# Optimization experiments

Hardware: AMD Instinct MI355X
Metric: run time of the kernel (lower is better)

Reference implementation:

```python
import jax, jax.numpy as jnp
import numpy as np
import math

VOCAB = 32000
DIM = 1024
TOKENS = 4096
PAD_IDX = 0
NBITS = 4
QN = -(2 ** (NBITS - 1))        # -8
QP = 2 ** (NBITS - 1) - 1       # 7


def setup_inputs() -> dict:
    key = jax.random.key(0)
    k_idx, k_w = jax.random.split(key)
    idx = jax.random.randint(k_idx, (TOKENS,), 0, VOCAB)
    # x is one-hot over the vocabulary, as implied by topk(x,1)[1] extracting the index
    x = jax.nn.one_hot(idx, VOCAB, dtype=jnp.float32)
    weight = jax.random.normal(k_w, (DIM, VOCAB), dtype=jnp.float32) * 0.02
    # LSQ init rule: alpha = 2 * mean|W| / sqrt(Qp)
    alpha = (2.0 * jnp.mean(jnp.abs(weight)) / math.sqrt(QP)).reshape(1)
    return {"x": x, "weight": weight, "alpha": alpha}


def reference(x, weight, alpha):
    # topk(x, 1)[1] on a one-hot input == argmax over vocab
    idx = jnp.argmax(x, axis=-1)                       # [T]
    mask = (idx == PAD_IDX)[:, None]                   # [T, 1]
    a = alpha[0]
    # LSQ fake-quantize the weight: round(clamp(w/alpha, Qn, Qp)) * alpha
    w_q = jnp.round(jnp.clip(weight / a, QN, QP)) * a  # [DIM, VOCAB]
    out = jnp.einsum('tv,dv->td', x, w_q)              # [T, DIM]
    return jnp.where(mask, 0.0, out)
```

## Files before the change

### kernel.cpp

```cpp
#include <hip/hip_runtime.h>


constexpr int VOCAB  = 32000;
constexpr int DIM    = 1024;
constexpr int TOKENS = 4096;
constexpr int V4     = VOCAB / 4;
constexpr int BLOCK  = 256;

__global__ __launch_bounds__(BLOCK) void emb_lsq_kernel(
    const float* __restrict__ x,
    const float* __restrict__ w,
    const float* __restrict__ alpha,
    float* __restrict__ out)
{
    const int t   = blockIdx.x;
    const int tid = threadIdx.x;

    __shared__ volatile int s_idx;
    if (tid == 0) s_idx = -1;
    __syncthreads();

    const float4* xr = reinterpret_cast<const float4*>(x + (size_t)t * VOCAB);
    for (int i = tid; i < V4; i += BLOCK) {
        float4 v = xr[i];
        int found = -1;
        if      (v.x > 0.5f) found = 4 * i + 0;
        else if (v.y > 0.5f) found = 4 * i + 1;
        else if (v.z > 0.5f) found = 4 * i + 2;
        else if (v.w > 0.5f) found = 4 * i + 3;
        if (found >= 0) s_idx = found;
        if (s_idx >= 0) break;
    }
    __syncthreads();
    const int idx = s_idx;

    float* orow = out + (size_t)t * DIM;
    if (idx == 0) {
        for (int d = tid; d < DIM; d += BLOCK) orow[d] = 0.0f;
    } else {
        const float a = alpha[0];
        for (int d = tid; d < DIM; d += BLOCK) {
            float wv = w[(size_t)d * VOCAB + idx];
            float q  = rintf(fminf(fmaxf(wv / a, -8.0f), 7.0f)) * a;
            orow[d]  = q;
        }
    }
}

extern "C" void kernel_launch(void* const* d_in, const int* in_sizes, int n_in,
                              void* d_out, int out_size, void* d_ws, size_t ws_size,
                              hipStream_t stream) {
    const float* x     = (const float*)d_in[0];
    const float* w     = (const float*)d_in[1];
    const float* alpha = (const float*)d_in[2];
    float* out         = (float*)d_out;

    emb_lsq_kernel<<<TOKENS, BLOCK, 0, stream>>>(x, w, alpha, out);
}
```

Before: 733.7 us.

## Use one wavefront per token with ballot-based early exit and unrolled loads

Each token is now handled by a single 64-lane wavefront instead of a 256-thread block. The one-hot search uses four-way unrolled vector loads per lane and a wave ballot for early exit, replacing the shared-memory flag and block barriers. The gather of weight values is unrolled into 16 independent loads per lane, and the output is written with vector stores. The aim is to drop synchronization overhead and get more memory-level parallelism per lane. The cost is fewer threads per token, so the scan over the x row gets less parallelism within each token.

```diff
diff --git a/kernel.cpp b/kernel.cpp
--- a/kernel.cpp
+++ b/kernel.cpp
@@ -1,48 +1,80 @@
 #include <hip/hip_runtime.h>
 
+
+typedef float v4f __attribute__((ext_vector_type(4)));
 
 constexpr int VOCAB  = 32000;
 constexpr int DIM    = 1024;
 constexpr int TOKENS = 4096;
 constexpr int V4     = VOCAB / 4;
-constexpr int BLOCK  = 256;
+constexpr int WAVE   = 64;
+constexpr int FULL_ITERS = V4 / 256;
+constexpr int TAIL_BASE  = FULL_ITERS * 256;
 
-__global__ __launch_bounds__(BLOCK) void emb_lsq_kernel(
+__device__ __forceinline__ int check4(v4f v, int chunk) {
+    if (v.x > 0.5f) return 4 * chunk + 0;
+    if (v.y > 0.5f) return 4 * chunk + 1;
+    if (v.z > 0.5f) return 4 * chunk + 2;
+    if (v.w > 0.5f) return 4 * chunk + 3;
+    return -1;
+}
+
+__global__ __launch_bounds__(WAVE) void emb_lsq_kernel(
     const float* __restrict__ x,
     const float* __restrict__ w,
     const float* __restrict__ alpha,
     float* __restrict__ out)
 {
-    const int t   = blockIdx.x;
-    const int tid = threadIdx.x;
+    const int t    = blockIdx.x;
+    const int lane = threadIdx.x;
 
-    __shared__ volatile int s_idx;
-    if (tid == 0) s_idx = -1;
-    __syncthreads();
+    const v4f* xr = reinterpret_cast<const v4f*>(x + (size_t)t * VOCAB);
+    int found = -1;
+    for (int k = 0; k < FULL_ITERS; ++k) {
+        const int i = lane + 256 * k;
+        v4f a0 = xr[i];
+        v4f a1 = xr[i +  64];
+        v4f a2 = xr[i + 128];
+        v4f a3 = xr[i + 192];
+        int f;
+        if ((f = check4(a0, i      )) >= 0) found = f;
+        else if ((f = check4(a1, i +  64)) >= 0) found = f;
+        else if ((f = check4(a2, i + 128)) >= 0) found = f;
+        else if ((f = check4(a3, i + 192)) >= 0) found = f;
+        if (__ballot(found >= 0)) break;
+    }
+    if (!__ballot(found >= 0)) {
+        v4f a = xr[TAIL_BASE + lane];
+        found = check4(a, TAIL_BASE + lane);
+    }
+    unsigned long long m = __ballot(found >= 0);
+    const int idx = m ? __shfl(found, (int)__ffsll(m) - 1) : -1;
 
-    const float4* xr = reinterpret_cast<const float4*>(x + (size_t)t * VOCAB);
-    for (int i = tid; i < V4; i += BLOCK) {
-        float4 v = xr[i];
-        int found = -1;
-        if      (v.x > 0.5f) found = 4 * i + 0;
-        else if (v.y > 0.5f) found = 4 * i + 1;
-        else if (v.z > 0.5f) found = 4 * i + 2;
-        else if (v.w > 0.5f) found = 4 * i + 3;
-        if (found >= 0) s_idx = found;
-        if (s_idx >= 0) break;
-    }
-    __syncthreads();
-    const int idx = s_idx;
-
-    float* orow = out + (size_t)t * DIM;
-    if (idx == 0) {
-        for (int d = tid; d < DIM; d += BLOCK) orow[d] = 0.0f;
+    v4f* orow = reinterpret_cast<v4f*>(out + (size_t)t * DIM);
+    if (idx <= 0) {
+        v4f z = 0.f;
+        #pragma unroll
+        for (int j = 0; j < 4; ++j) orow[lane + 64 * j] = z;
     } else {
         const float a = alpha[0];
-        for (int d = tid; d < DIM; d += BLOCK) {
-            float wv = w[(size_t)d * VOCAB + idx];
-            float q  = rintf(fminf(fmaxf(wv / a, -8.0f), 7.0f)) * a;
-            orow[d]  = q;
+        const size_t col = (size_t)idx;
+        float wv[16];
+        #pragma unroll
+        for (int j = 0; j < 4; ++j) {
+            const int d0 = 4 * lane + 256 * j;
+            wv[4*j+0] = w[(size_t)(d0 + 0) * VOCAB + col];
+            wv[4*j+1] = w[(size_t)(d0 + 1) * VOCAB + col];
+            wv[4*j+2] = w[(size_t)(d0 + 2) * VOCAB + col];
+            wv[4*j+3] = w[(size_t)(d0 + 3) * VOCAB + col];
+        }
+        #pragma unroll
+        for (int j = 0; j < 4; ++j) {
+            v4f q;
+            q.x = rintf(fminf(fmaxf(wv[4*j+0] / a, -8.f), 7.f)) * a;
+            q.y = rintf(fminf(fmaxf(wv[4*j+1] / a, -8.f), 7.f)) * a;
+            q.z = rintf(fminf(fmaxf(wv[4*j+2] / a, -8.f), 7.f)) * a;
+            q.w = rintf(fminf(fmaxf(wv[4*j+3] / a, -8.f), 7.f)) * a;
+            orow[lane + 64 * j] = q;
         }
     }
 }
@@ -55,5 +87,5 @@
     const float* alpha = (const float*)d_in[2];
     float* out         = (float*)d_out;
 
-    emb_lsq_kernel<<<TOKENS, BLOCK, 0, stream>>>(x, w, alpha, out);
+    emb_lsq_kernel<<<TOKENS, WAVE, 0, stream>>>(x, w, alpha, out);
 }
```

After: 719.8 us. Within noise of the previous version (-1.9%).
